# Performance work log

Hardware: AMD Instinct MI355X
Metric: run time of the kernel (lower is better)

The kernel has to match this reference:

```python
import jax, jax.numpy as jnp
import numpy as np

CD_WEIGHT = 100.0


def setup_inputs() -> dict:
    key = jax.random.key(0)
    k1, k2 = jax.random.split(key)
    array1 = jax.random.normal(k1, (4, 4096, 3), dtype=jnp.float32)
    array2 = jax.random.normal(k2, (4, 4096, 3), dtype=jnp.float32)
    return {"array1": array1, "array2": array2}


def _chamfer(a1, a2):
    # a1: [B, N, D], a2: [B, M, D]
    # squared pairwise distances d2[b, n, m] = ||a1[b,n] - a2[b,m]||^2
    # computed as ||a||^2 + ||b||^2 - 2 a.b to avoid materializing [B,N,M,D]
    sq1 = jnp.sum(a1 * a1, axis=-1)                      # [B, N]
    sq2 = jnp.sum(a2 * a2, axis=-1)                      # [B, M]
    cross = jnp.einsum("bnd,bmd->bnm", a1, a2)           # [B, N, M]
    d2 = sq1[:, :, None] + sq2[:, None, :] - 2.0 * cross  # [B, N, M]
    # av_dist1: for each array2 point, min over array1 points, then mean
    av_dist1 = jnp.mean(jnp.min(d2, axis=1), axis=-1)    # [B]
    # av_dist2: for each array1 point, min over array2 points, then mean
    av_dist2 = jnp.mean(jnp.min(d2, axis=2), axis=-1)    # [B]
    return CD_WEIGHT * jnp.mean(0.5 * (av_dist1 + av_dist2))


def reference(array1, array2):
    return _chamfer(array1, array2)
```

## Files before the change

### kernel.cpp

```cpp
#include <hip/hip_runtime.h>
#include <math.h>


#define NPTS     4096
#define NBATCH   4
#define RCHUNK   2048
#define QPB      256
#define QBLK     64
#define QPT      16
#define NSLICE   64
#define RSLICE   (RCHUNK / NSLICE)
#define SSTRIDE  33
#define NBLK     (2 * NBATCH * (NPTS / QBLK) * (NPTS / RCHUNK))
#define SCALE    (50.0f / (float)(NBATCH * NPTS))

__global__ __launch_bounds__(QPB, 4) void chamfer_main(
    const float* __restrict__ a1, const float* __restrict__ a2,
    unsigned int* __restrict__ gmin, float* __restrict__ out)
{
    __shared__ float4 refs[NSLICE * SSTRIDE];
    __shared__ float4 qlds[QBLK];
    __shared__ float  pm2[4][QBLK];

    const int bid  = blockIdx.x;
    const int qc   = bid & 63;
    const int b    = (bid >> 6) & 3;
    const int half = (bid >> 8) & 1;
    const int dir  = bid >> 9;
    const float* q = (dir == 0) ? a1 : a2;
    const float* r = (dir == 0) ? a2 : a1;
    q += (size_t)b * NPTS * 3 + (size_t)qc * QBLK * 3;
    r += (size_t)b * NPTS * 3 + (size_t)half * RCHUNK * 3;

    const int tid = threadIdx.x;

    if (bid == 0 && tid == 0) out[0] = 0.0f;

    for (int g = tid; g < RCHUNK; g += QPB) {
        float rx = r[3 * g + 0];
        float ry = r[3 * g + 1];
        float rz = r[3 * g + 2];
        refs[(g >> 5) * SSTRIDE + (g & 31)] =
            make_float4(rx, ry, rz, rx * rx + ry * ry + rz * rz);
    }
    if (tid < QBLK) {
        float x = q[3 * tid + 0];
        float y = q[3 * tid + 1];
        float z = q[3 * tid + 2];
        qlds[tid] = make_float4(-2.0f * x, -2.0f * y, -2.0f * z,
                                x * x + y * y + z * z);
    }
    __syncthreads();

    const int qg = (tid & 3) * QPT;
    const int s  = tid >> 2;
    float qx2[QPT], qy2[QPT], qz2[QPT];
    #pragma unroll
    for (int k = 0; k < QPT; ++k) {
        float4 ql = qlds[qg + k];
        qx2[k] = ql.x; qy2[k] = ql.y; qz2[k] = ql.z;
    }

    float mins[QPT];
    #pragma unroll
    for (int k = 0; k < QPT; ++k) mins[k] = INFINITY;

    const float4* rp = &refs[s * SSTRIDE];
    #pragma unroll 2
    for (int j = 0; j < RSLICE; ++j) {
        float4 p = rp[j];
        #pragma unroll
        for (int k = 0; k < QPT; ++k) {
            float t = fmaf(qz2[k], p.z,
                      fmaf(qy2[k], p.y,
                      fmaf(qx2[k], p.x, p.w)));
            mins[k] = fminf(mins[k], t);
        }
    }

    #pragma unroll
    for (int m = 4; m <= 32; m <<= 1) {
        #pragma unroll
        for (int k = 0; k < QPT; ++k)
            mins[k] = fminf(mins[k], __shfl_xor(mins[k], m));
    }
    const int wv = tid >> 6;
    if ((tid & 63) < 4) {
        #pragma unroll
        for (int k = 0; k < QPT; ++k)
            pm2[wv][qg + k] = mins[k];
    }
    __syncthreads();

    if (tid < QBLK) {
        float m = fminf(fminf(pm2[0][tid], pm2[1][tid]),
                        fminf(pm2[2][tid], pm2[3][tid]));
        float d2 = fmaxf(m + qlds[tid].w, 0.0f);
        const int qidx = (dir * NBATCH + b) * NPTS + qc * QBLK + tid;
        atomicMin(&gmin[qidx], __float_as_uint(d2));
    }
}

__global__ __launch_bounds__(256) void chamfer_final(
    const unsigned int* __restrict__ gmin, float* __restrict__ out)
{
    const int i = blockIdx.x * 512 + threadIdx.x;
    float s = __uint_as_float(gmin[i]) + __uint_as_float(gmin[i + 256]);
    for (int off = 32; off > 0; off >>= 1) s += __shfl_down(s, off);
    __shared__ float wsum[4];
    if ((threadIdx.x & 63) == 0) wsum[threadIdx.x >> 6] = s;
    __syncthreads();
    if (threadIdx.x == 0)
        atomicAdd(out, (wsum[0] + wsum[1] + wsum[2] + wsum[3]) * SCALE);
}

extern "C" void kernel_launch(void* const* d_in, const int* in_sizes, int n_in,
                              void* d_out, int out_size, void* d_ws, size_t ws_size,
                              hipStream_t stream) {
    const float* a1 = (const float*)d_in[0];
    const float* a2 = (const float*)d_in[1];
    float* out = (float*)d_out;
    unsigned int* gmin = (unsigned int*)d_ws;

    chamfer_main<<<NBLK, QPB, 0, stream>>>(a1, a2, gmin, out);
    chamfer_final<<<2 * NBATCH * NPTS / 512, 256, 0, stream>>>(gmin, out);
}
```

Measured before the change: 72.16 us.

## Prepack points into float4 with norms in a separate pre-kernel

Adds a pack kernel that converts both point arrays into float4 (x,y,z,|p|^2) in workspace once, so each main block loads reference and query tiles with coalesced float4 loads rather than re-reading strided xyz and recomputing norms. The inner loop is manually unrolled to process two reference points per iteration, and the final reduction uses 1024-thread blocks with a two-level shuffle. It adds a third kernel launch and an extra pass through global memory, and moves the output zeroing into the pack kernel.

```diff
diff --git a/kernel.cpp b/kernel.cpp
--- a/kernel.cpp
+++ b/kernel.cpp
@@ -4,19 +4,33 @@
 
 #define NPTS     4096
 #define NBATCH   4
-#define RCHUNK   2048
 #define QPB      256
 #define QBLK     64
 #define QPT      16
+#define RCHUNK   2048
 #define NSLICE   64
 #define RSLICE   (RCHUNK / NSLICE)
 #define SSTRIDE  33
-#define NBLK     (2 * NBATCH * (NPTS / QBLK) * (NPTS / RCHUNK))
+#define NBLK     (2 * NBATCH * (NPTS / QBLK) * 2)
+#define NQTOT    (NBATCH * NPTS)
 #define SCALE    (50.0f / (float)(NBATCH * NPTS))
 
+__global__ __launch_bounds__(256) void chamfer_pack(
+    const float* __restrict__ a1, const float* __restrict__ a2,
+    float4* __restrict__ pk, float* __restrict__ out)
+{
+    const int idx = blockIdx.x * 256 + threadIdx.x;
+    if (idx == 0) out[0] = 0.0f;
+    const float* src = (idx < NQTOT) ? a1 : a2;
+    const int i = idx & (NQTOT - 1);
+    float x = src[3 * i + 0];
+    float y = src[3 * i + 1];
+    float z = src[3 * i + 2];
+    pk[idx] = make_float4(x, y, z, x * x + y * y + z * z);
+}
+
 __global__ __launch_bounds__(QPB, 4) void chamfer_main(
-    const float* __restrict__ a1, const float* __restrict__ a2,
-    unsigned int* __restrict__ gmin, float* __restrict__ out)
+    const float4* __restrict__ pk, unsigned int* __restrict__ gmin)
 {
     __shared__ float4 refs[NSLICE * SSTRIDE];
     __shared__ float4 qlds[QBLK];
@@ -27,29 +41,17 @@
     const int b    = (bid >> 6) & 3;
     const int half = (bid >> 8) & 1;
     const int dir  = bid >> 9;
-    const float* q = (dir == 0) ? a1 : a2;
-    const float* r = (dir == 0) ? a2 : a1;
-    q += (size_t)b * NPTS * 3 + (size_t)qc * QBLK * 3;
-    r += (size_t)b * NPTS * 3 + (size_t)half * RCHUNK * 3;
+    const float4* qp = pk + (dir == 0 ? 0 : NQTOT) + b * NPTS + qc * QBLK;
+    const float4* rg = pk + (dir == 0 ? NQTOT : 0) + b * NPTS + half * RCHUNK;
 
     const int tid = threadIdx.x;
 
-    if (bid == 0 && tid == 0) out[0] = 0.0f;
-
-    for (int g = tid; g < RCHUNK; g += QPB) {
-        float rx = r[3 * g + 0];
-        float ry = r[3 * g + 1];
-        float rz = r[3 * g + 2];
-        refs[(g >> 5) * SSTRIDE + (g & 31)] =
-            make_float4(rx, ry, rz, rx * rx + ry * ry + rz * rz);
+    #pragma unroll
+    for (int i = 0; i < RCHUNK / QPB; ++i) {
+        const int g = tid + i * QPB;
+        refs[(g >> 5) * SSTRIDE + (g & 31)] = rg[g];
     }
-    if (tid < QBLK) {
-        float x = q[3 * tid + 0];
-        float y = q[3 * tid + 1];
-        float z = q[3 * tid + 2];
-        qlds[tid] = make_float4(-2.0f * x, -2.0f * y, -2.0f * z,
-                                x * x + y * y + z * z);
-    }
+    if (tid < QBLK) qlds[tid] = qp[tid];
     __syncthreads();
 
     const int qg = (tid & 3) * QPT;
@@ -58,7 +60,7 @@
     #pragma unroll
     for (int k = 0; k < QPT; ++k) {
         float4 ql = qlds[qg + k];
-        qx2[k] = ql.x; qy2[k] = ql.y; qz2[k] = ql.z;
+        qx2[k] = -2.0f * ql.x; qy2[k] = -2.0f * ql.y; qz2[k] = -2.0f * ql.z;
     }
 
     float mins[QPT];
@@ -67,14 +69,18 @@
 
     const float4* rp = &refs[s * SSTRIDE];
     #pragma unroll 2
-    for (int j = 0; j < RSLICE; ++j) {
-        float4 p = rp[j];
+    for (int j = 0; j < RSLICE; j += 2) {
+        float4 p0 = rp[j];
+        float4 p1 = rp[j + 1];
         #pragma unroll
         for (int k = 0; k < QPT; ++k) {
-            float t = fmaf(qz2[k], p.z,
-                      fmaf(qy2[k], p.y,
-                      fmaf(qx2[k], p.x, p.w)));
-            mins[k] = fminf(mins[k], t);
+            float t0 = fmaf(qz2[k], p0.z,
+                       fmaf(qy2[k], p0.y,
+                       fmaf(qx2[k], p0.x, p0.w)));
+            float t1 = fmaf(qz2[k], p1.z,
+                       fmaf(qy2[k], p1.y,
+                       fmaf(qx2[k], p1.x, p1.w)));
+            mins[k] = fminf(mins[k], fminf(t0, t1));
         }
     }
 
@@ -101,17 +107,20 @@
     }
 }
 
-__global__ __launch_bounds__(256) void chamfer_final(
+__global__ __launch_bounds__(1024) void chamfer_final(
     const unsigned int* __restrict__ gmin, float* __restrict__ out)
 {
-    const int i = blockIdx.x * 512 + threadIdx.x;
-    float s = __uint_as_float(gmin[i]) + __uint_as_float(gmin[i + 256]);
+    const int i = blockIdx.x * 1024 + threadIdx.x;
+    float s = __uint_as_float(gmin[i]);
     for (int off = 32; off > 0; off >>= 1) s += __shfl_down(s, off);
-    __shared__ float wsum[4];
+    __shared__ float wsum[16];
     if ((threadIdx.x & 63) == 0) wsum[threadIdx.x >> 6] = s;
     __syncthreads();
-    if (threadIdx.x == 0)
-        atomicAdd(out, (wsum[0] + wsum[1] + wsum[2] + wsum[3]) * SCALE);
+    if (threadIdx.x < 64) {
+        float v = (threadIdx.x < 16) ? wsum[threadIdx.x] : 0.0f;
+        for (int off = 8; off > 0; off >>= 1) v += __shfl_down(v, off);
+        if (threadIdx.x == 0) atomicAdd(out, v * SCALE);
+    }
 }
 
 extern "C" void kernel_launch(void* const* d_in, const int* in_sizes, int n_in,
@@ -121,7 +130,9 @@
     const float* a2 = (const float*)d_in[1];
     float* out = (float*)d_out;
     unsigned int* gmin = (unsigned int*)d_ws;
+    float4* pk = (float4*)((char*)d_ws + 131072);
 
-    chamfer_main<<<NBLK, QPB, 0, stream>>>(a1, a2, gmin, out);
-    chamfer_final<<<2 * NBATCH * NPTS / 512, 256, 0, stream>>>(gmin, out);
+    chamfer_pack<<<2 * NQTOT / 256, 256, 0, stream>>>(a1, a2, pk, out);
+    chamfer_main<<<NBLK, QPB, 0, stream>>>(pk, gmin);
+    chamfer_final<<<2 * NQTOT / 1024, 1024, 0, stream>>>(gmin, out);
 }
```

After: 73.48 us. About the same (+1.8%).
